# Kernel tuning notes

Hardware: AMD Instinct MI355X
Metric: run time of the kernel (lower is better)

## Reference

```python
import jax, jax.numpy as jnp
import numpy as np

B, N, F, UNITS = 8, 4096, 128, 64
NEG = -1e10
LEAKY_SLOPE = 0.2  # tf.nn.leaky_relu default


def setup_inputs() -> dict:
    key = jax.random.key(0)
    k1, k2, k3, k4, k5 = jax.random.split(key, 5)
    H = jax.random.normal(k1, (B, N, F), dtype=jnp.float32)
    A = jax.random.randint(k2, (B, N, N), 0, 2).astype(jnp.float32)
    # self-loops so every row has at least one unmasked entry
    A = jnp.maximum(A, jnp.eye(N, dtype=jnp.float32)[None])
    W = jax.random.normal(k3, (F, UNITS), dtype=jnp.float32) * (1.0 / np.sqrt(F))
    a_1 = jax.random.normal(k4, (UNITS, 1), dtype=jnp.float32) * (1.0 / np.sqrt(UNITS))
    a_2 = jax.random.normal(k5, (UNITS, 1), dtype=jnp.float32) * (1.0 / np.sqrt(UNITS))
    return {"H": H, "A": A, "W": W, "a_1": a_1, "a_2": a_2}


def reference(H, A, W, a_1, a_2):
    X = H @ W                                  # [B, N, U]
    attn_self = X @ a_1                        # [B, N, 1]
    attn_neigh = X @ a_2                       # [B, N, 1]
    attention = attn_self + jnp.swapaxes(attn_neigh, 1, 2)   # [B, N, N]
    E = jax.nn.leaky_relu(attention, negative_slope=LEAKY_SLOPE)
    masked_E = E + NEG * (1.0 - A)
    alpha = jax.nn.softmax(masked_E, axis=-1)  # row-wise softmax
    H_cap = alpha @ X                          # [B, N, U]
    return jax.nn.relu(H_cap)
```

## Files before the change

### kernel.cpp

```cpp
#include <hip/hip_runtime.h>
#include <hip/hip_bf16.h>


#define NTOK 4096
#define FDIM 128
#define UDIM 64
#define BATCH 8

typedef __attribute__((ext_vector_type(8))) short short8;
typedef __attribute__((ext_vector_type(4))) float f32x4;

union PackU { unsigned u[4]; short8 s; };

__device__ __forceinline__ unsigned short f2bf(float x) {
    unsigned u = __float_as_uint(x);
    return (unsigned short)((u + 0x7fffu + ((u >> 16) & 1u)) >> 16);
}

__global__ __launch_bounds__(256) void prep_kernel(
    const float* __restrict__ H,
    const float* __restrict__ W,
    const float* __restrict__ a1,
    const float* __restrict__ a2,
    unsigned short* __restrict__ XT,
    float* __restrict__ s_out,
    float* __restrict__ t_out)
{
    __shared__ float Xl[4][16][UDIM + 1];

    const int tid  = threadIdx.x;
    const int wave = tid >> 6, lane = tid & 63;
    const int col  = lane & 15, quad = lane >> 4;
    const int i0   = (blockIdx.x * 4 + wave) * 16;

    f32x4 acc0 = {0,0,0,0}, acc1 = {0,0,0,0}, acc2 = {0,0,0,0}, acc3 = {0,0,0,0};
    const float* hrow = H + (size_t)(i0 + col) * FDIM + quad * 8;

    #pragma unroll
    for (int kb = 0; kb < FDIM; kb += 32) {
        f32x4 h0 = *(const f32x4*)(hrow + kb);
        f32x4 h1 = *(const f32x4*)(hrow + kb + 4);
        short8 afr, b0, b1, b2, b3;
        #pragma unroll
        for (int j = 0; j < 4; ++j) {
            afr[j]     = (short)f2bf(h0[j]);
            afr[4 + j] = (short)f2bf(h1[j]);
        }
        #pragma unroll
        for (int j = 0; j < 8; ++j) {
            int k = kb + quad * 8 + j;
            b0[j] = (short)f2bf(W[k * UDIM + col]);
            b1[j] = (short)f2bf(W[k * UDIM + 16 + col]);
            b2[j] = (short)f2bf(W[k * UDIM + 32 + col]);
            b3[j] = (short)f2bf(W[k * UDIM + 48 + col]);
        }
        acc0 = __builtin_amdgcn_mfma_f32_16x16x32_bf16(afr, b0, acc0, 0, 0, 0);
        acc1 = __builtin_amdgcn_mfma_f32_16x16x32_bf16(afr, b1, acc1, 0, 0, 0);
        acc2 = __builtin_amdgcn_mfma_f32_16x16x32_bf16(afr, b2, acc2, 0, 0, 0);
        acc3 = __builtin_amdgcn_mfma_f32_16x16x32_bf16(afr, b3, acc3, 0, 0, 0);
    }
    #pragma unroll
    for (int r = 0; r < 4; ++r) {
        Xl[wave][quad * 4 + r][col]      = acc0[r];
        Xl[wave][quad * 4 + r][16 + col] = acc1[r];
        Xl[wave][quad * 4 + r][32 + col] = acc2[r];
        Xl[wave][quad * 4 + r][48 + col] = acc3[r];
    }
    __syncthreads();

    const int b = i0 >> 12, n0 = i0 & (NTOK - 1);
    float ps = 0.f, pt = 0.f;
    #pragma unroll
    for (int ui = 0; ui < 16; ++ui) {
        int u = quad * 16 + ui;
        float x = Xl[wave][col][u];
        ps = fmaf(x, a1[u], ps);
        pt = fmaf(x, a2[u], pt);
    }
    ps += __shfl_xor(ps, 16, 64); ps += __shfl_xor(ps, 32, 64);
    pt += __shfl_xor(pt, 16, 64); pt += __shfl_xor(pt, 32, 64);
    const float LOG2E = 1.44269504f;
    if (quad == 0) s_out[i0 + col] = ps * LOG2E;
    if (quad == 1) t_out[i0 + col] = pt * LOG2E;

    #pragma unroll
    for (int ui = 0; ui < 16; ++ui) {
        int u = quad * 16 + ui;
        XT[(size_t)(b * UDIM + u) * NTOK + n0 + col] = f2bf(Xl[wave][col][u]);
    }
}

__global__ __launch_bounds__(256) void attn_kernel(
    const float* __restrict__ A,
    const unsigned short* __restrict__ XT,
    const float* __restrict__ s_in,
    const float* __restrict__ t_in,
    float* __restrict__ out)
{
    __shared__ float part[4][64][UDIM + 1];
    __shared__ float denl[4][64];

    const int tid  = threadIdx.x;
    const int wave = tid >> 6, lane = tid & 63;
    const int bx   = blockIdx.x;
    const int b    = bx & 7;
    const int i0   = (bx >> 3) * 64;
    const int col  = lane & 15, quad = lane >> 4;
    const int kstart = wave * (NTOK / 4);

    float s_m[4];
    #pragma unroll
    for (int g = 0; g < 4; ++g) s_m[g] = s_in[b * NTOK + i0 + g * 16 + col];

    const float* ap[4];
    #pragma unroll
    for (int g = 0; g < 4; ++g)
        ap[g] = A + ((size_t)(b * NTOK + i0 + g * 16 + col)) * NTOK + kstart + quad * 8;
    const float* tptr = t_in + b * NTOK + kstart + quad * 8;
    const unsigned short* xb  = XT + (size_t)b * UDIM * NTOK + kstart + quad * 8;
    const unsigned short* xp0 = xb + (size_t)(col)      * NTOK;
    const unsigned short* xp1 = xb + (size_t)(16 + col) * NTOK;
    const unsigned short* xp2 = xb + (size_t)(32 + col) * NTOK;
    const unsigned short* xp3 = xb + (size_t)(48 + col) * NTOK;

    f32x4 acc[4][4];
    #pragma unroll
    for (int g = 0; g < 4; ++g)
        #pragma unroll
        for (int f = 0; f < 4; ++f) acc[g][f] = (f32x4){0,0,0,0};
    float den[4] = {0.f, 0.f, 0.f, 0.f};

    #pragma unroll 2
    for (int step = 0; step < 32; ++step) {
        short8 bf0 = *(const short8*)xp0;
        short8 bf1 = *(const short8*)xp1;
        short8 bf2 = *(const short8*)xp2;
        short8 bf3 = *(const short8*)xp3;
        f32x4 t0  = *(const f32x4*)tptr;
        f32x4 t1  = *(const f32x4*)(tptr + 4);

        #pragma unroll
        for (int g = 0; g < 4; ++g) {
            f32x4 am0 = __builtin_nontemporal_load((const f32x4*)ap[g]);
            f32x4 am1 = __builtin_nontemporal_load((const f32x4*)(ap[g] + 4));
            unsigned uw[8];
            #pragma unroll
            for (int j = 0; j < 4; ++j) {
                float l0 = s_m[g] + t0[j], l1 = s_m[g] + t1[j];
                float e0 = fmaxf(l0, 0.2f * l0);
                float e1 = fmaxf(l1, 0.2f * l1);
                float w0 = __builtin_amdgcn_exp2f(e0) * am0[j];
                float w1 = __builtin_amdgcn_exp2f(e1) * am1[j];
                den[g] += w0 + w1;
                uw[j]     = __float_as_uint(w0) + 0x8000u;
                uw[4 + j] = __float_as_uint(w1) + 0x8000u;
            }
            PackU p;
            p.u[0] = __builtin_amdgcn_perm(uw[1], uw[0], 0x07060302u);
            p.u[1] = __builtin_amdgcn_perm(uw[3], uw[2], 0x07060302u);
            p.u[2] = __builtin_amdgcn_perm(uw[5], uw[4], 0x07060302u);
            p.u[3] = __builtin_amdgcn_perm(uw[7], uw[6], 0x07060302u);

            acc[g][0] = __builtin_amdgcn_mfma_f32_16x16x32_bf16(p.s, bf0, acc[g][0], 0, 0, 0);
            acc[g][1] = __builtin_amdgcn_mfma_f32_16x16x32_bf16(p.s, bf1, acc[g][1], 0, 0, 0);
            acc[g][2] = __builtin_amdgcn_mfma_f32_16x16x32_bf16(p.s, bf2, acc[g][2], 0, 0, 0);
            acc[g][3] = __builtin_amdgcn_mfma_f32_16x16x32_bf16(p.s, bf3, acc[g][3], 0, 0, 0);
            ap[g] += 32;
        }
        tptr += 32; xp0 += 32; xp1 += 32; xp2 += 32; xp3 += 32;
    }

    #pragma unroll
    for (int g = 0; g < 4; ++g) {
        den[g] += __shfl_xor(den[g], 16, 64);
        den[g] += __shfl_xor(den[g], 32, 64);
        if (quad == 0) denl[wave][g * 16 + col] = den[g];
        #pragma unroll
        for (int r = 0; r < 4; ++r) {
            part[wave][g * 16 + quad * 4 + r][col]      = acc[g][0][r];
            part[wave][g * 16 + quad * 4 + r][16 + col] = acc[g][1][r];
            part[wave][g * 16 + quad * 4 + r][32 + col] = acc[g][2][r];
            part[wave][g * 16 + quad * 4 + r][48 + col] = acc[g][3][r];
        }
    }
    __syncthreads();

    #pragma unroll
    for (int rep = 0; rep < 16; ++rep) {
        int e = rep * 256 + tid;
        int r = e >> 6, u = e & 63;
        float num = part[0][r][u] + part[1][r][u] + part[2][r][u] + part[3][r][u];
        float dd  = denl[0][r] + denl[1][r] + denl[2][r] + denl[3][r];
        float o   = fmaxf(num / dd, 0.f);
        __builtin_nontemporal_store(o, &out[(size_t)(b * NTOK + i0 + r) * UDIM + u]);
    }
}

extern "C" void kernel_launch(void* const* d_in, const int* in_sizes, int n_in,
                              void* d_out, int out_size, void* d_ws, size_t ws_size,
                              hipStream_t stream) {
    const float* H  = (const float*)d_in[0];
    const float* A  = (const float*)d_in[1];
    const float* W  = (const float*)d_in[2];
    const float* a1 = (const float*)d_in[3];
    const float* a2 = (const float*)d_in[4];
    float* out = (float*)d_out;

    char* ws = (char*)d_ws;
    unsigned short* XT = (unsigned short*)ws;
    float* s = (float*)(ws + (size_t)BATCH * UDIM * NTOK * 2);
    float* t = (float*)(ws + (size_t)BATCH * UDIM * NTOK * 2 + (size_t)BATCH * NTOK * 4);

    prep_kernel<<<512, 256, 0, stream>>>(H, W, a1, a2, XT, s, t);
    attn_kernel<<<512, 256, 0, stream>>>(A, XT, s, t, out);
}
```

Before: 741.3 us.

## Precompress adjacency matrix to byte mask before attention kernel

Extra blocks are added to the prep kernel. They stream the fp32 adjacency matrix once and write a one-byte-per-entry mask into the workspace. The attention kernel then reads 8 bytes of mask per lane per step instead of two 16-byte fp32 vectors, cutting its A-load traffic by four. The aim is to ease the memory-latency pressure of the main loop. In exchange, the prep stage now reads the full matrix and writes a 128 MB mask, so total DRAM traffic goes up.

```diff
diff --git a/kernel.cpp b/kernel.cpp
--- a/kernel.cpp
+++ b/kernel.cpp
@@ -17,16 +17,45 @@
     return (unsigned short)((u + 0x7fffu + ((u >> 16) & 1u)) >> 16);
 }
 
+#define PREP_BLOCKS 512
+#define CMP_BLOCKS 2048
 __global__ __launch_bounds__(256) void prep_kernel(
     const float* __restrict__ H,
     const float* __restrict__ W,
     const float* __restrict__ a1,
     const float* __restrict__ a2,
+    const float* __restrict__ A,
     unsigned short* __restrict__ XT,
     float* __restrict__ s_out,
-    float* __restrict__ t_out)
+    float* __restrict__ t_out,
+    unsigned char* __restrict__ AM)
 {
     __shared__ float Xl[4][16][UDIM + 1];
+
+    if (blockIdx.x >= PREP_BLOCKS) {
+        const size_t tidg = (size_t)(blockIdx.x - PREP_BLOCKS) * 256 + threadIdx.x;
+        const size_t STR  = (size_t)CMP_BLOCKS * 256;
+        const f32x4* av = (const f32x4*)A;
+        unsigned* mw = (unsigned*)AM;
+        #pragma unroll 1
+        for (int it = 0; it < 32; ++it) {
+            size_t w0 = tidg + (size_t)(2 * it) * STR;
+            size_t w1 = w0 + STR;
+            f32x4 v0 = __builtin_nontemporal_load(av + w0);
+            f32x4 v1 = __builtin_nontemporal_load(av + w1);
+            unsigned m0 = (v0[0] != 0.f ? 1u : 0u)
+                        | (v0[1] != 0.f ? 1u << 8 : 0u)
+                        | (v0[2] != 0.f ? 1u << 16 : 0u)
+                        | (v0[3] != 0.f ? 1u << 24 : 0u);
+            unsigned m1 = (v1[0] != 0.f ? 1u : 0u)
+                        | (v1[1] != 0.f ? 1u << 8 : 0u)
+                        | (v1[2] != 0.f ? 1u << 16 : 0u)
+                        | (v1[3] != 0.f ? 1u << 24 : 0u);
+            mw[w0] = m0;
+            mw[w1] = m1;
+        }
+        return;
+    }
 
     const int tid  = threadIdx.x;
     const int wave = tid >> 6, lane = tid & 63;
@@ -91,7 +120,7 @@
 }
 
 __global__ __launch_bounds__(256) void attn_kernel(
-    const float* __restrict__ A,
+    const unsigned char* __restrict__ AM,
     const unsigned short* __restrict__ XT,
     const float* __restrict__ s_in,
     const float* __restrict__ t_in,
@@ -112,10 +141,10 @@
     #pragma unroll
     for (int g = 0; g < 4; ++g) s_m[g] = s_in[b * NTOK + i0 + g * 16 + col];
 
-    const float* ap[4];
+    const unsigned char* mp[4];
     #pragma unroll
     for (int g = 0; g < 4; ++g)
-        ap[g] = A + ((size_t)(b * NTOK + i0 + g * 16 + col)) * NTOK + kstart + quad * 8;
+        mp[g] = AM + ((size_t)(b * NTOK + i0 + g * 16 + col)) * NTOK + kstart + quad * 8;
     const float* tptr = t_in + b * NTOK + kstart + quad * 8;
     const unsigned short* xb  = XT + (size_t)b * UDIM * NTOK + kstart + quad * 8;
     const unsigned short* xp0 = xb + (size_t)(col)      * NTOK;
@@ -141,16 +170,17 @@
 
         #pragma unroll
         for (int g = 0; g < 4; ++g) {
-            f32x4 am0 = __builtin_nontemporal_load((const f32x4*)ap[g]);
-            f32x4 am1 = __builtin_nontemporal_load((const f32x4*)(ap[g] + 4));
+            uint2 mv = *(const uint2*)mp[g];
             unsigned uw[8];
             #pragma unroll
             for (int j = 0; j < 4; ++j) {
+                float am0 = (float)((mv.x >> (8 * j)) & 0xffu);
+                float am1 = (float)((mv.y >> (8 * j)) & 0xffu);
                 float l0 = s_m[g] + t0[j], l1 = s_m[g] + t1[j];
                 float e0 = fmaxf(l0, 0.2f * l0);
                 float e1 = fmaxf(l1, 0.2f * l1);
-                float w0 = __builtin_amdgcn_exp2f(e0) * am0[j];
-                float w1 = __builtin_amdgcn_exp2f(e1) * am1[j];
+                float w0 = __builtin_amdgcn_exp2f(e0) * am0;
+                float w1 = __builtin_amdgcn_exp2f(e1) * am1;
                 den[g] += w0 + w1;
                 uw[j]     = __float_as_uint(w0) + 0x8000u;
                 uw[4 + j] = __float_as_uint(w1) + 0x8000u;
@@ -165,7 +195,7 @@
             acc[g][1] = __builtin_amdgcn_mfma_f32_16x16x32_bf16(p.s, bf1, acc[g][1], 0, 0, 0);
             acc[g][2] = __builtin_amdgcn_mfma_f32_16x16x32_bf16(p.s, bf2, acc[g][2], 0, 0, 0);
             acc[g][3] = __builtin_amdgcn_mfma_f32_16x16x32_bf16(p.s, bf3, acc[g][3], 0, 0, 0);
-            ap[g] += 32;
+            mp[g] += 32;
         }
         tptr += 32; xp0 += 32; xp1 += 32; xp2 += 32; xp3 += 32;
     }
@@ -208,9 +238,13 @@
 
     char* ws = (char*)d_ws;
     unsigned short* XT = (unsigned short*)ws;
-    float* s = (float*)(ws + (size_t)BATCH * UDIM * NTOK * 2);
-    float* t = (float*)(ws + (size_t)BATCH * UDIM * NTOK * 2 + (size_t)BATCH * NTOK * 4);
-
-    prep_kernel<<<512, 256, 0, stream>>>(H, W, a1, a2, XT, s, t);
-    attn_kernel<<<512, 256, 0, stream>>>(A, XT, s, t, out);
-}
+    size_t off = (size_t)BATCH * UDIM * NTOK * 2;
+    float* s = (float*)(ws + off);
+    off += (size_t)BATCH * NTOK * 4;
+    float* t = (float*)(ws + off);
+    off += (size_t)BATCH * NTOK * 4;
+    unsigned char* AM = (unsigned char*)(ws + off);
+
+    prep_kernel<<<PREP_BLOCKS + CMP_BLOCKS, 256, 0, stream>>>(H, W, a1, a2, A, XT, s, t, AM);
+    attn_kernel<<<512, 256, 0, stream>>>(AM, XT, s, t, out);
+}
```

Result: slower. 764.5 us (+3.1%).

## Stage A and X tiles through double-buffered LDS with per-wave row ownership

Applied to the files above, without the earlier changes.

The attention kernel now has the block cooperatively load 64x64 tiles of A and of the transposed X into double-buffered shared memory, prefetching the next tile into registers while computing the current one. Each wave owns 16 rows across the whole key range instead of splitting keys four ways, so the cross-wave partial-sum reduction through LDS goes away and the wave writes its output directly. The aim is fully coalesced A reads and X reuse across waves, at the price of a barrier per 64-key step and extra LDS traffic for the fp32 A tile.

```diff
diff --git a/kernel.cpp b/kernel.cpp
--- a/kernel.cpp
+++ b/kernel.cpp
@@ -6,6 +6,7 @@
 #define FDIM 128
 #define UDIM 64
 #define BATCH 8
+#define BK 64
 
 typedef __attribute__((ext_vector_type(8))) short short8;
 typedef __attribute__((ext_vector_type(4))) float f32x4;
@@ -97,61 +98,73 @@
     const float* __restrict__ t_in,
     float* __restrict__ out)
 {
-    __shared__ float part[4][64][UDIM + 1];
-    __shared__ float denl[4][64];
+    __shared__ __align__(16) float          As[2][64][BK + 4];
+    __shared__ __align__(16) unsigned short Xs[2][64][BK + 8];
 
     const int tid  = threadIdx.x;
     const int wave = tid >> 6, lane = tid & 63;
-    const int bx   = blockIdx.x;
-    const int b    = bx & 7;
-    const int i0   = (bx >> 3) * 64;
     const int col  = lane & 15, quad = lane >> 4;
-    const int kstart = wave * (NTOK / 4);
-
-    float s_m[4];
-    #pragma unroll
-    for (int g = 0; g < 4; ++g) s_m[g] = s_in[b * NTOK + i0 + g * 16 + col];
-
-    const float* ap[4];
-    #pragma unroll
-    for (int g = 0; g < 4; ++g)
-        ap[g] = A + ((size_t)(b * NTOK + i0 + g * 16 + col)) * NTOK + kstart + quad * 8;
-    const float* tptr = t_in + b * NTOK + kstart + quad * 8;
-    const unsigned short* xb  = XT + (size_t)b * UDIM * NTOK + kstart + quad * 8;
-    const unsigned short* xp0 = xb + (size_t)(col)      * NTOK;
-    const unsigned short* xp1 = xb + (size_t)(16 + col) * NTOK;
-    const unsigned short* xp2 = xb + (size_t)(32 + col) * NTOK;
-    const unsigned short* xp3 = xb + (size_t)(48 + col) * NTOK;
-
-    f32x4 acc[4][4];
-    #pragma unroll
-    for (int g = 0; g < 4; ++g)
-        #pragma unroll
-        for (int f = 0; f < 4; ++f) acc[g][f] = (f32x4){0,0,0,0};
-    float den[4] = {0.f, 0.f, 0.f, 0.f};
-
-    #pragma unroll 2
-    for (int step = 0; step < 32; ++step) {
-        short8 bf0 = *(const short8*)xp0;
-        short8 bf1 = *(const short8*)xp1;
-        short8 bf2 = *(const short8*)xp2;
-        short8 bf3 = *(const short8*)xp3;
-        f32x4 t0  = *(const f32x4*)tptr;
-        f32x4 t1  = *(const f32x4*)(tptr + 4);
-
-        #pragma unroll
-        for (int g = 0; g < 4; ++g) {
-            f32x4 am0 = __builtin_nontemporal_load((const f32x4*)ap[g]);
-            f32x4 am1 = __builtin_nontemporal_load((const f32x4*)(ap[g] + 4));
+    const int b    = blockIdx.x & 7;
+    const int i0   = (blockIdx.x >> 3) * 64;
+
+    const int arow = tid >> 4, acol = (tid & 15) * 4;
+    const int xrow = tid >> 3, xcol = (tid & 7) * 8;
+    const float* agp = A + ((size_t)(b * NTOK + i0 + arow)) * NTOK + acol;
+    const unsigned short* xgp = XT + ((size_t)(b * UDIM + xrow)) * NTOK + xcol;
+
+    const float s_m = s_in[b * NTOK + i0 + wave * 16 + col];
+    const float* tbase = t_in + b * NTOK;
+
+    f32x4 acc[4];
+    #pragma unroll
+    for (int f = 0; f < 4; ++f) acc[f] = (f32x4){0,0,0,0};
+    float den = 0.f;
+
+    f32x4 av[4], xv[2];
+
+    #pragma unroll
+    for (int i = 0; i < 4; ++i)
+        av[i] = __builtin_nontemporal_load((const f32x4*)(agp + (size_t)i * 16 * NTOK));
+    #pragma unroll
+    for (int i = 0; i < 2; ++i)
+        xv[i] = *(const f32x4*)(xgp + (size_t)i * 32 * NTOK);
+    #pragma unroll
+    for (int i = 0; i < 4; ++i) *(f32x4*)&As[0][arow + i * 16][acol] = av[i];
+    #pragma unroll
+    for (int i = 0; i < 2; ++i) *(f32x4*)&Xs[0][xrow + i * 32][xcol] = xv[i];
+
+    for (int c = 0; c < NTOK / BK; ++c) {
+        const int buf = c & 1;
+        if (c < NTOK / BK - 1) {
+            const float* ag = agp + (c + 1) * BK;
+            const unsigned short* xg = xgp + (c + 1) * BK;
+            #pragma unroll
+            for (int i = 0; i < 4; ++i)
+                av[i] = __builtin_nontemporal_load((const f32x4*)(ag + (size_t)i * 16 * NTOK));
+            #pragma unroll
+            for (int i = 0; i < 2; ++i)
+                xv[i] = *(const f32x4*)(xg + (size_t)i * 32 * NTOK);
+        }
+        __syncthreads();
+
+        #pragma unroll
+        for (int ks = 0; ks < 2; ++ks) {
+            const float* ar = &As[buf][wave * 16 + col][ks * 32 + quad * 8];
+            f32x4 a0 = *(const f32x4*)ar;
+            f32x4 a1 = *(const f32x4*)(ar + 4);
+            const float* tp = tbase + c * BK + ks * 32 + quad * 8;
+            f32x4 t0 = *(const f32x4*)tp;
+            f32x4 t1 = *(const f32x4*)(tp + 4);
+
             unsigned uw[8];
             #pragma unroll
             for (int j = 0; j < 4; ++j) {
-                float l0 = s_m[g] + t0[j], l1 = s_m[g] + t1[j];
+                float l0 = s_m + t0[j], l1 = s_m + t1[j];
                 float e0 = fmaxf(l0, 0.2f * l0);
                 float e1 = fmaxf(l1, 0.2f * l1);
-                float w0 = __builtin_amdgcn_exp2f(e0) * am0[j];
-                float w1 = __builtin_amdgcn_exp2f(e1) * am1[j];
-                den[g] += w0 + w1;
+                float w0 = __builtin_amdgcn_exp2f(e0) * a0[j];
+                float w1 = __builtin_amdgcn_exp2f(e1) * a1[j];
+                den += w0 + w1;
                 uw[j]     = __float_as_uint(w0) + 0x8000u;
                 uw[4 + j] = __float_as_uint(w1) + 0x8000u;
             }
@@ -161,38 +174,37 @@
             p.u[2] = __builtin_amdgcn_perm(uw[5], uw[4], 0x07060302u);
             p.u[3] = __builtin_amdgcn_perm(uw[7], uw[6], 0x07060302u);
 
-            acc[g][0] = __builtin_amdgcn_mfma_f32_16x16x32_bf16(p.s, bf0, acc[g][0], 0, 0, 0);
-            acc[g][1] = __builtin_amdgcn_mfma_f32_16x16x32_bf16(p.s, bf1, acc[g][1], 0, 0, 0);
-            acc[g][2] = __builtin_amdgcn_mfma_f32_16x16x32_bf16(p.s, bf2, acc[g][2], 0, 0, 0);
-            acc[g][3] = __builtin_amdgcn_mfma_f32_16x16x32_bf16(p.s, bf3, acc[g][3], 0, 0, 0);
-            ap[g] += 32;
-        }
-        tptr += 32; xp0 += 32; xp1 += 32; xp2 += 32; xp3 += 32;
-    }
-
-    #pragma unroll
-    for (int g = 0; g < 4; ++g) {
-        den[g] += __shfl_xor(den[g], 16, 64);
-        den[g] += __shfl_xor(den[g], 32, 64);
-        if (quad == 0) denl[wave][g * 16 + col] = den[g];
-        #pragma unroll
-        for (int r = 0; r < 4; ++r) {
-            part[wave][g * 16 + quad * 4 + r][col]      = acc[g][0][r];
-            part[wave][g * 16 + quad * 4 + r][16 + col] = acc[g][1][r];
-            part[wave][g * 16 + quad * 4 + r][32 + col] = acc[g][2][r];
-            part[wave][g * 16 + quad * 4 + r][48 + col] = acc[g][3][r];
-        }
-    }
-    __syncthreads();
-
-    #pragma unroll
-    for (int rep = 0; rep < 16; ++rep) {
-        int e = rep * 256 + tid;
-        int r = e >> 6, u = e & 63;
-        float num = part[0][r][u] + part[1][r][u] + part[2][r][u] + part[3][r][u];
-        float dd  = denl[0][r] + denl[1][r] + denl[2][r] + denl[3][r];
-        float o   = fmaxf(num / dd, 0.f);
-        __builtin_nontemporal_store(o, &out[(size_t)(b * NTOK + i0 + r) * UDIM + u]);
+            short8 bf0 = *(const short8*)&Xs[buf][col]     [ks * 32 + quad * 8];
+            short8 bf1 = *(const short8*)&Xs[buf][16 + col][ks * 32 + quad * 8];
+            short8 bf2 = *(const short8*)&Xs[buf][32 + col][ks * 32 + quad * 8];
+            short8 bf3 = *(const short8*)&Xs[buf][48 + col][ks * 32 + quad * 8];
+
+            acc[0] = __builtin_amdgcn_mfma_f32_16x16x32_bf16(p.s, bf0, acc[0], 0, 0, 0);
+            acc[1] = __builtin_amdgcn_mfma_f32_16x16x32_bf16(p.s, bf1, acc[1], 0, 0, 0);
+            acc[2] = __builtin_amdgcn_mfma_f32_16x16x32_bf16(p.s, bf2, acc[2], 0, 0, 0);
+            acc[3] = __builtin_amdgcn_mfma_f32_16x16x32_bf16(p.s, bf3, acc[3], 0, 0, 0);
+        }
+
+        if (c < NTOK / BK - 1) {
+            const int nb = buf ^ 1;
+            #pragma unroll
+            for (int i = 0; i < 4; ++i) *(f32x4*)&As[nb][arow + i * 16][acol] = av[i];
+            #pragma unroll
+            for (int i = 0; i < 2; ++i) *(f32x4*)&Xs[nb][xrow + i * 32][xcol] = xv[i];
+        }
+    }
+
+    den += __shfl_xor(den, 16, 64);
+    den += __shfl_xor(den, 32, 64);
+    #pragma unroll
+    for (int r = 0; r < 4; ++r) {
+        float dd = __shfl(den, quad * 4 + r, 64);
+        const int row = i0 + wave * 16 + quad * 4 + r;
+        #pragma unroll
+        for (int f = 0; f < 4; ++f) {
+            float o = fmaxf(acc[f][r] / dd, 0.f);
+            __builtin_nontemporal_store(o, &out[(size_t)(b * NTOK + row) * UDIM + f * 16 + col]);
+        }
     }
 }
 
@@ -208,8 +220,10 @@
 
     char* ws = (char*)d_ws;
     unsigned short* XT = (unsigned short*)ws;
-    float* s = (float*)(ws + (size_t)BATCH * UDIM * NTOK * 2);
-    float* t = (float*)(ws + (size_t)BATCH * UDIM * NTOK * 2 + (size_t)BATCH * NTOK * 4);
+    size_t off = (size_t)BATCH * UDIM * NTOK * 2;
+    float* s = (float*)(ws + off);
+    off += (size_t)BATCH * NTOK * 4;
+    float* t = (float*)(ws + off);
 
     prep_kernel<<<512, 256, 0, stream>>>(H, W, a1, a2, XT, s, t);
     attn_kernel<<<512, 256, 0, stream>>>(A, XT, s, t, out);
```

Result: faster. 702.4 us, median of 3 (-5.2%).
